# Optimization experiments

Hardware: AMD Instinct MI355X
Metric: run time of the kernel (lower is better)

## Reference

```python
import jax, jax.numpy as jnp
import numpy as np

TIME_GAP_BUCKETS = 64
B, L, H, MAX_T = 256, 200, 256, 256
VOCAB, N_GROUPS = 50000, 16
EPS = 1e-5


def setup_inputs() -> dict:
    key = jax.random.key(0)
    ks = jax.random.split(key, 16)
    lengths = jax.random.randint(ks[0], (B,), 0, L + 1)
    mask = jnp.arange(L)[None, :] < lengths[:, None]

    def toks(k, hi):  # jagged padded-dense: zeros past each row's length
        return jnp.where(mask, jax.random.randint(k, (B, L), 0, hi), 0)

    inp = {
        'history_tokens': toks(ks[1], VOCAB),
        'history_post_tokens': toks(ks[2], VOCAB),
        'history_author_tokens': toks(ks[3], VOCAB),
        'history_action_tokens': toks(ks[4], VOCAB),
        'history_time_gap': toks(ks[5], TIME_GAP_BUCKETS + 1),
        'history_group_ids': jnp.where(mask, jnp.sort(jax.random.randint(ks[6], (B, L), 1, N_GROUPS + 1), axis=1), 0),
        'lengths': lengths,
    }
    s = 0.02
    inp['token_emb'] = jax.random.normal(ks[7], (VOCAB, H)) * s
    inp['ln_gamma'] = jnp.ones((6 * H,))
    inp['ln_beta'] = jnp.zeros((6 * H,))
    inp['w1'] = jax.random.normal(ks[8], (6 * H, 4 * H)) * (1.0 / np.sqrt(6 * H)).astype(np.float32)
    inp['b1'] = jnp.zeros((4 * H,))
    inp['w2'] = jax.random.normal(ks[9], (4 * H, H)) * (1.0 / np.sqrt(4 * H)).astype(np.float32)
    inp['b2'] = jnp.zeros((H,))
    inp['time_gap_emb'] = (jax.random.normal(ks[10], (TIME_GAP_BUCKETS + 1, H)) * s).at[0].set(0.0)  # padding_idx=0
    inp['group_emb'] = (jax.random.normal(ks[11], (N_GROUPS + 1, H)) * s).at[0].set(0.0)  # padding_idx=0
    inp['pos_emb'] = jax.random.normal(ks[12], (MAX_T, H)) * s
    inp['sep_token'] = jax.random.normal(ks[13], (H,)) * 0.02
    return inp


def _layernorm(x, g, b):
    mu = jnp.mean(x, axis=-1, keepdims=True)
    var = jnp.mean(jnp.square(x - mu), axis=-1, keepdims=True)
    return (x - mu) * jax.lax.rsqrt(var + EPS) * g + b


def _merge_with_sep(event_tokens, group_ids, mask, sep_token):
    # mask is a prefix mask (positions < lengths), so valid tokens are contiguous.
    Bn, Ln, Hn = event_tokens.shape
    next_mask = jnp.pad(mask[:, 1:], ((0, 0), (0, 1)))
    next_group = jnp.pad(group_ids[:, 1:], ((0, 0), (0, 1)))
    sep_after = mask & next_mask & (group_ids != next_group)  # insert sep after token i
    seps_before = jnp.cumsum(sep_after, axis=1) - sep_after.astype(jnp.int32)  # exclusive scan
    token_pos = jnp.arange(Ln)[None, :] + seps_before  # position within merged piece list
    total = mask.sum(axis=1) + sep_after.sum(axis=1)  # [B] merged piece count
    offset = MAX_T - total  # right-align; negative -> leading pieces dropped
    tok_idx = offset[:, None] + token_pos
    sep_idx = tok_idx + 1
    tok_idx = jnp.where(mask & (tok_idx >= 0), tok_idx, MAX_T)  # MAX_T => dropped
    sep_idx = jnp.where(sep_after & (sep_idx >= 0), sep_idx, MAX_T)
    sep_rows = jnp.broadcast_to(sep_token, (Ln, Hn))

    def scatter_one(ev, ti, si):
        buf = jnp.zeros((MAX_T, Hn), ev.dtype)
        buf = buf.at[ti].set(ev, mode='drop')
        buf = buf.at[si].set(sep_rows, mode='drop')
        return buf

    merged = jax.vmap(scatter_one)(event_tokens, tok_idx, sep_idx)
    merged_len = jnp.minimum(total, MAX_T)
    merged_mask = jnp.arange(MAX_T)[None, :] >= (MAX_T - merged_len)[:, None]
    return merged, merged_mask


def reference(history_tokens, history_post_tokens, history_author_tokens,
              history_action_tokens, history_time_gap, history_group_ids,
              lengths, token_emb, ln_gamma, ln_beta, w1, b1, w2, b2,
              time_gap_emb, group_emb, pos_emb, sep_token):
    mask = jnp.arange(L)[None, :] < lengths[:, None]
    hh = token_emb[history_tokens]
    ph = token_emb[history_post_tokens]
    ah = token_emb[history_author_tokens]
    ch = token_emb[history_action_tokens]
    th = time_gap_emb[jnp.clip(history_time_gap, 0, TIME_GAP_BUCKETS)]
    gh = group_emb[history_group_ids]
    ev = jnp.concatenate([hh, ph, ah, ch, th, gh], axis=-1)  # [B, L, 6H]
    x = _layernorm(ev, ln_gamma, ln_beta)
    x = jax.nn.silu(x @ w1 + b1)  # dropout is identity in eval mode
    event_tokens = x @ w2 + b2  # [B, L, H]
    merged, mm = _merge_with_sep(event_tokens, history_group_ids, mask, sep_token)
    merged = (merged + pos_emb[None]) * mm[..., None].astype(merged.dtype)
    return merged, mm
```

## Files before the change

### kernel.cpp

```cpp
#include <hip/hip_runtime.h>
#include <hip/hip_bf16.h>
#include <math.h>

#define B_    256
#define L_    200
#define H_    256
#define MAXT  256
#define SIXH  1536
#define FOURH 1024
#define NPOS  (B_ * L_)

typedef __attribute__((ext_vector_type(8))) short short8;
typedef __attribute__((ext_vector_type(4))) float f32x4;

typedef __attribute__((address_space(3))) void lds_void;
typedef const __attribute__((address_space(1))) void gbl_void;

#define ASM_BAR() asm volatile("s_barrier" ::: "memory")
#define VMCNT4()  asm volatile("s_waitcnt vmcnt(4)" ::: "memory")
#define VMCNT0()  asm volatile("s_waitcnt vmcnt(0)" ::: "memory")

__global__ void fused_pre(const int* __restrict__ lengths,
                          const int* __restrict__ gids,
                          int* __restrict__ offsets,
                          int* __restrict__ tpos,
                          __hip_bfloat16* __restrict__ x) {
  int b = blockIdx.x, t = threadIdx.x;
  int lane = t & 63, wv = t >> 6;

  int len_t = lengths[t];
  int s = len_t;
#pragma unroll
  for (int o = 1; o < 64; o <<= 1) {
    int v = __shfl_up(s, o);
    if (lane >= o) s += v;
  }
  __shared__ int wsum[4];
  __shared__ int all_off[257];
  if (lane == 63) wsum[wv] = s;
  __syncthreads();
  int pre = 0;
#pragma unroll
  for (int k = 0; k < 4; k++)
    if (k < wv) pre += wsum[k];
  s += pre;
  all_off[t] = s - len_t;
  if (t == 255) all_off[256] = s;
  __syncthreads();

  int base = all_off[b];
  int total = all_off[256];
  if (t == 0) {
    offsets[b] = base;
    if (b == 0) offsets[B_] = total;
  }

  __shared__ int g[L_];
  int len = lengths[b];
  for (int l = t; l < len; l += 256) g[l] = gids[b * L_ + l];
  __syncthreads();
  if (t == 0) {
    int nsep = 0;
    for (int l = 0; l + 1 < len; l++)
      if (g[l] != g[l + 1]) nsep++;
    int tot = len + nsep;
    int off = MAXT - tot;
    int sb = 0;
    for (int l = 0; l < len; l++) {
      int ti = off + l + sb;
      tpos[base + l] = (ti >= 0) ? (b * MAXT + ti) : -1;
      if (l + 1 < len && g[l] != g[l + 1]) sb++;
    }
  }

  int padded = (total + 255) & ~255;
  int row = total + b;
  if (row < padded) {
#pragma unroll
    for (int j = 0; j < 6; j++)
      x[(size_t)row * SIXH + j * 256 + t] = __float2bfloat16(0.0f);
  }
}

__global__ void transpose_both(const float* __restrict__ w1,
                               __hip_bfloat16* __restrict__ w1t,
                               const float* __restrict__ w2,
                               __hip_bfloat16* __restrict__ w2t) {
  __shared__ float tile[32][33];
  int id = blockIdx.x;
  const float* in; __hip_bfloat16* out; int R, C, tc, tr;
  if (id < 1536) {
    in = w1; out = w1t; R = 1536; C = 1024; tc = id & 31; tr = id >> 5;
  } else {
    int j = id - 1536;
    in = w2; out = w2t; R = 1024; C = 256; tc = j & 7; tr = j >> 3;
  }
  int tx = threadIdx.x & 31, ty = threadIdx.x >> 5;
#pragma unroll
  for (int i = 0; i < 4; i++)
    tile[ty + i * 8][tx] = in[(size_t)(tr * 32 + ty + i * 8) * C + tc * 32 + tx];
  __syncthreads();
#pragma unroll
  for (int i = 0; i < 4; i++)
    out[(size_t)(tc * 32 + ty + i * 8) * R + tr * 32 + tx] =
        __float2bfloat16(tile[tx][ty + i * 8]);
}

__global__ void embed_ln_kernel(const int* __restrict__ tok0,
                                const int* __restrict__ tok1,
                                const int* __restrict__ tok2,
                                const int* __restrict__ tok3,
                                const int* __restrict__ tgap,
                                const int* __restrict__ gid,
                                const int* __restrict__ lengths,
                                const int* __restrict__ offsets,
                                const float* __restrict__ token_emb,
                                const float* __restrict__ tg_emb,
                                const float* __restrict__ g_emb,
                                const float* __restrict__ gamma,
                                const float* __restrict__ beta,
                                __hip_bfloat16* __restrict__ xout) {
  int l = blockIdx.x, b = blockIdx.y;
  if (l >= lengths[b]) return;
  int pos = b * L_ + l;
  int row = offsets[b] + l;
  int t = threadIdx.x;
  int wv = t >> 6;
  int ln = t & 63;
  int c4 = ln * 4;

  const float* tab;
  int idx;
  if (wv == 0)      { tab = token_emb; idx = tok0[pos]; }
  else if (wv == 1) { tab = token_emb; idx = tok1[pos]; }
  else if (wv == 2) { tab = token_emb; idx = tok2[pos]; }
  else if (wv == 3) { tab = token_emb; idx = tok3[pos]; }
  else if (wv == 4) { tab = tg_emb;    idx = min(max(tgap[pos], 0), 64); }
  else              { tab = g_emb;     idx = gid[pos]; }

  float4 v = *(const float4*)&tab[(size_t)idx * H_ + c4];

  float s = v.x + v.y + v.z + v.w;
  float q = v.x * v.x + v.y * v.y + v.z * v.z + v.w * v.w;
#pragma unroll
  for (int o = 32; o; o >>= 1) { s += __shfl_down(s, o); q += __shfl_down(q, o); }
  __shared__ float ps[6], pq[6];
  if (ln == 0) { ps[wv] = s; pq[wv] = q; }
  __syncthreads();
  float ts = 0.f, tq = 0.f;
#pragma unroll
  for (int k = 0; k < 6; k++) { ts += ps[k]; tq += pq[k]; }
  float mu = ts * (1.0f / 1536.0f);
  float var = tq * (1.0f / 1536.0f) - mu * mu;
  float rstd = rsqrtf(var + 1e-5f);

  int cbase = wv * 256 + c4;
  float4 gm = *(const float4*)&gamma[cbase];
  float4 bt = *(const float4*)&beta[cbase];
  float y0 = (v.x - mu) * rstd * gm.x + bt.x;
  float y1 = (v.y - mu) * rstd * gm.y + bt.y;
  float y2 = (v.z - mu) * rstd * gm.z + bt.z;
  float y3 = (v.w - mu) * rstd * gm.w + bt.w;
  __hip_bfloat16 h0 = __float2bfloat16(y0), h1 = __float2bfloat16(y1);
  __hip_bfloat16 h2 = __float2bfloat16(y2), h3 = __float2bfloat16(y3);
  ushort4 pk;
  pk.x = *(unsigned short*)&h0; pk.y = *(unsigned short*)&h1;
  pk.z = *(unsigned short*)&h2; pk.w = *(unsigned short*)&h3;
  *(ushort4*)&xout[(size_t)row * SIXH + cbase] = pk;
}

__global__ __launch_bounds__(512, 2)
void gemm1_8ph(const __hip_bfloat16* __restrict__ A,
               const __hip_bfloat16* __restrict__ Bt,
               const float* __restrict__ bias,
               __hip_bfloat16* __restrict__ out,
               const int* __restrict__ total_ptr) {
  constexpr int K = SIXH;
  constexpr int NT = K / 64;
  constexpr int N = FOURH;

  extern __shared__ __align__(16) char lds[];

  int total = total_ptr[0];
  int padded = (total + 255) & ~255;
  int num_mt = padded >> 8;

  int bid = blockIdx.x;
  int xcd = bid & 7;
  int slot = bid >> 3;
  int nt = slot & 3;
  int mtb = slot >> 2;
  int n0 = nt * 256;

  int tid = threadIdx.x;
  int lane = tid & 63;
  int w = tid >> 6;
  int wave_m = w >> 2;
  int wave_n = w & 3;

  int r15 = lane & 15, g = lane >> 4;
  int slot_r = (((r15 & 1) << 2) | g) ^ (r15 >> 1);
  int lane_off = (r15 >> 1) * 128 + slot_r * 16;

  int s0 = (tid & 7) ^ ((tid >> 3) & 7);
  int scol = (s0 & 3) * 8;
  int row0 = ((tid >> 3) << 1) + (s0 >> 2);
  int ldst0 = w * 1024;

  float bv4[4];
#pragma unroll
  for (int ni = 0; ni < 4; ni++)
    bv4[ni] = bias[n0 + wave_n * 64 + ni * 16 + r15];

#define REGA(d, h) (lds + (d) * 65536 + (h) * 16384)
#define REGB(d, h) (lds + (d) * 65536 + 32768 + (h) * 16384)

#define STAGE(P, t0, kt, h, rb)                                                \
  do {                                                                         \
    __builtin_amdgcn_global_load_lds(                                          \
        (gbl_void*)((P) + (size_t)((t0) + row0) * K + (kt) * 64 + (h) * 32 +   \
                    scol),                                                     \
        (lds_void*)((rb) + ldst0), 16, 0, 0);                                  \
    __builtin_amdgcn_global_load_lds(                                          \
        (gbl_void*)((P) + (size_t)((t0) + row0 + 128) * K + (kt) * 64 +        \
                    (h) * 32 + scol),                                          \
        (lds_void*)((rb) + 8192 + ldst0), 16, 0, 0);                           \
  } while (0)

  for (int mt = xcd + 8 * mtb; mt < num_mt; mt += 64) {
    int m0 = mt * 256;

    f32x4 acc[8][4] = {};

    STAGE(A, m0, 0, 0, REGA(0, 0));
    STAGE(Bt, n0, 0, 0, REGB(0, 0));
    STAGE(A, m0, 0, 1, REGA(0, 1));
    STAGE(Bt, n0, 0, 1, REGB(0, 1));
    STAGE(A, m0, 1, 0, REGA(1, 0));
    STAGE(Bt, n0, 1, 0, REGB(1, 0));
    VMCNT4();
    ASM_BAR();

    for (int kt = 0; kt < NT; ++kt) {
      int d = kt & 1;
      int kc1 = (kt + 1 < NT) ? kt + 1 : NT - 1;
      int kc2 = (kt + 2 < NT) ? kt + 2 : NT - 1;
      char* A0 = REGA(d, 0); char* A1 = REGA(d, 1);
      char* B0 = REGB(d, 0); char* B1 = REGB(d, 1);
      char* An1 = REGA(d ^ 1, 1);
      char* Bn1 = REGB(d ^ 1, 1);

      short8 a[4], b[4];

#pragma unroll
      for (int ni = 0; ni < 4; ni++)
        b[ni] = *(const short8*)(B0 + (wave_n * 64 + ni * 16) * 64 + lane_off);
#pragma unroll
      for (int j = 0; j < 4; j++)
        a[j] = *(const short8*)(A0 + (wave_m * 128 + j * 16) * 64 + lane_off);
      STAGE(A, m0, kc1, 1, An1);
      __builtin_amdgcn_s_setprio(1);
#pragma unroll
      for (int j = 0; j < 4; j++)
#pragma unroll
        for (int ni = 0; ni < 4; ni++)
          acc[j][ni] = __builtin_amdgcn_mfma_f32_16x16x32_bf16(a[j], b[ni],
                                                               acc[j][ni], 0, 0, 0);
      __builtin_amdgcn_s_setprio(0);
#pragma unroll
      for (int j = 0; j < 4; j++)
        a[j] = *(const short8*)(A0 + (wave_m * 128 + (4 + j) * 16) * 64 + lane_off);
      STAGE(Bt, n0, kc1, 1, Bn1);
      __builtin_amdgcn_s_setprio(1);
#pragma unroll
      for (int j = 0; j < 4; j++)
#pragma unroll
        for (int ni = 0; ni < 4; ni++)
          acc[4 + j][ni] = __builtin_amdgcn_mfma_f32_16x16x32_bf16(
              a[j], b[ni], acc[4 + j][ni], 0, 0, 0);
      __builtin_amdgcn_s_setprio(0);
      ASM_BAR();

#pragma unroll
      for (int ni = 0; ni < 4; ni++)
        b[ni] = *(const short8*)(B1 + (wave_n * 64 + ni * 16) * 64 + lane_off);
#pragma unroll
      for (int j = 0; j < 4; j++)
        a[j] = *(const short8*)(A1 + (wave_m * 128 + j * 16) * 64 + lane_off);
      STAGE(A, m0, kc2, 0, A0);
      __builtin_amdgcn_s_setprio(1);
#pragma unroll
      for (int j = 0; j < 4; j++)
#pragma unroll
        for (int ni = 0; ni < 4; ni++)
          acc[j][ni] = __builtin_amdgcn_mfma_f32_16x16x32_bf16(a[j], b[ni],
                                                               acc[j][ni], 0, 0, 0);
      __builtin_amdgcn_s_setprio(0);
#pragma unroll
      for (int j = 0; j < 4; j++)
        a[j] = *(const short8*)(A1 + (wave_m * 128 + (4 + j) * 16) * 64 + lane_off);
      STAGE(Bt, n0, kc2, 0, B0);
      __builtin_amdgcn_s_setprio(1);
#pragma unroll
      for (int j = 0; j < 4; j++)
#pragma unroll
        for (int ni = 0; ni < 4; ni++)
          acc[4 + j][ni] = __builtin_amdgcn_mfma_f32_16x16x32_bf16(
              a[j], b[ni], acc[4 + j][ni], 0, 0, 0);
      __builtin_amdgcn_s_setprio(0);
      VMCNT4();
      ASM_BAR();
    }
    VMCNT0();

    int r0 = g * 4;
#pragma unroll
    for (int mi = 0; mi < 8; mi++)
#pragma unroll
      for (int ni = 0; ni < 4; ni++) {
        int col = n0 + wave_n * 64 + ni * 16 + r15;
        float bv = bv4[ni];
#pragma unroll
        for (int r = 0; r < 4; r++) {
          int row = m0 + wave_m * 128 + mi * 16 + r0 + r;
          float v = acc[mi][ni][r] + bv;
          v = v / (1.0f + __expf(-v));
          out[(size_t)row * N + col] = __float2bfloat16(v);
        }
      }
  }
#undef STAGE
#undef REGA
#undef REGB
}

__global__ __launch_bounds__(512, 2)
void gemm2_wide(const __hip_bfloat16* __restrict__ A,
                const __hip_bfloat16* __restrict__ Bt,
                const float* __restrict__ bias,
                const int* __restrict__ tpos,
                const float* __restrict__ pos_emb,
                float* __restrict__ out,
                const int* __restrict__ total_ptr) {
  constexpr int K = FOURH;
  int m0 = blockIdx.x * 128;
  int total = total_ptr[0];
  int padded = (total + 127) & ~127;
  if (m0 >= padded) return;

  __shared__ __hip_bfloat16 As[128 * 64];
  __shared__ __hip_bfloat16 Bs[256 * 64];
  int tid = threadIdx.x;
  int lane = tid & 63, w = tid >> 6;
  int wave_m = w >> 2;
  int wave_n = w & 3;
  int wm = wave_m * 64, wn = wave_n * 64;

  int srow = lane >> 3;
  int scol = (lane & 7) * 8;
  int r15 = lane & 15, g = lane >> 4;

  f32x4 acc[4][4] = {};

  for (int k0 = 0; k0 < K; k0 += 64) {
#pragma unroll
    for (int i = 0; i < 2; i++) {
      int c = w * 2 + i;
      int row = c * 8 + srow;
      __builtin_amdgcn_global_load_lds(
          (gbl_void*)&A[(size_t)(m0 + row) * K + k0 + scol],
          (lds_void*)(As + c * 512), 16, 0, 0);
    }
#pragma unroll
    for (int i = 0; i < 4; i++) {
      int c = w * 4 + i;
      int row = c * 8 + srow;
      __builtin_amdgcn_global_load_lds(
          (gbl_void*)&Bt[(size_t)row * K + k0 + scol],
          (lds_void*)(Bs + c * 512), 16, 0, 0);
    }
    __syncthreads();
#pragma unroll
    for (int kk = 0; kk < 64; kk += 32) {
      short8 a[4], bb[4];
#pragma unroll
      for (int m = 0; m < 4; m++)
        a[m] = *(const short8*)&As[(wm + m * 16 + r15) * 64 + kk + 8 * g];
#pragma unroll
      for (int n = 0; n < 4; n++)
        bb[n] = *(const short8*)&Bs[(wn + n * 16 + r15) * 64 + kk + 8 * g];
#pragma unroll
      for (int m = 0; m < 4; m++)
#pragma unroll
        for (int n = 0; n < 4; n++)
          acc[m][n] = __builtin_amdgcn_mfma_f32_16x16x32_bf16(a[m], bb[n],
                                                              acc[m][n], 0, 0, 0);
    }
    __syncthreads();
  }

  int r0 = g * 4;
#pragma unroll
  for (int m = 0; m < 4; m++) {
#pragma unroll
    for (int r = 0; r < 4; r++) {
      int row = m0 + wm + m * 16 + r0 + r;
      if (row >= total) continue;
      int pa = tpos[row];
      if (pa < 0) continue;
      int p = pa & (MAXT - 1);
#pragma unroll
      for (int n = 0; n < 4; n++) {
        int col = wn + n * 16 + r15;
        float v = acc[m][n][r] + bias[col] + pos_emb[p * H_ + col];
        out[(size_t)pa * H_ + col] = v;
      }
    }
  }
}

__global__ void merge2_kernel(const int* __restrict__ gids,
                              const int* __restrict__ lengths,
                              const float* __restrict__ sep_token,
                              const float* __restrict__ pos_emb,
                              float* __restrict__ out) {
  int b = blockIdx.x, t = threadIdx.x;
  __shared__ signed char src[MAXT];
  __shared__ int g[L_];
  __shared__ int sh_total;
  int len = lengths[b];
  src[t] = 0;
  for (int l = t; l < len; l += 256) g[l] = gids[b * L_ + l];
  __syncthreads();
  if (t == 0) {
    int nsep = 0;
    for (int l = 0; l + 1 < len; l++)
      if (g[l] != g[l + 1]) nsep++;
    int total = len + nsep;
    sh_total = total;
    int off = MAXT - total;
    int sb = 0;
    for (int l = 0; l < len; l++) {
      int ti = off + l + sb;
      if (ti >= 0) src[ti] = 2;
      if (l + 1 < len && g[l] != g[l + 1]) {
        if (ti + 1 >= 0) src[ti + 1] = 1;
        sb++;
      }
    }
  }
  __syncthreads();
  int total = sh_total;
  int mlen = min(total, MAXT);

  int q = t >> 6, lane = t & 63, c4 = lane * 4;
  float4 sep4 = *(const float4*)&sep_token[c4];
  float* orow = out + (size_t)b * MAXT * H_;
  for (int p0 = 0; p0 < MAXT; p0 += 4) {
    int p = p0 + q;
    int s = src[p];
    if (s == 2) continue;
    float4 v;
    if (s == 1) {
      float4 pe = *(const float4*)&pos_emb[p * H_ + c4];
      v.x = sep4.x + pe.x; v.y = sep4.y + pe.y;
      v.z = sep4.z + pe.z; v.w = sep4.w + pe.w;
    } else {
      v.x = 0.f; v.y = 0.f; v.z = 0.f; v.w = 0.f;
    }
    *(float4*)&orow[(size_t)p * H_ + c4] = v;
  }
  float* mm = out + (size_t)B_ * MAXT * H_;
  mm[b * MAXT + t] = (t >= MAXT - mlen) ? 1.0f : 0.0f;
}

extern "C" void kernel_launch(void* const* d_in, const int* in_sizes, int n_in,
                              void* d_out, int out_size, void* d_ws,
                              size_t ws_size, hipStream_t stream) {
  const int* tok0 = (const int*)d_in[0];
  const int* tok1 = (const int*)d_in[1];
  const int* tok2 = (const int*)d_in[2];
  const int* tok3 = (const int*)d_in[3];
  const int* tgap = (const int*)d_in[4];
  const int* gid  = (const int*)d_in[5];
  const int* lengths = (const int*)d_in[6];
  const float* token_emb = (const float*)d_in[7];
  const float* gamma = (const float*)d_in[8];
  const float* beta  = (const float*)d_in[9];
  const float* w1 = (const float*)d_in[10];
  const float* b1 = (const float*)d_in[11];
  const float* w2 = (const float*)d_in[12];
  const float* b2 = (const float*)d_in[13];
  const float* tg_emb = (const float*)d_in[14];
  const float* g_emb  = (const float*)d_in[15];
  const float* pos_emb = (const float*)d_in[16];
  const float* sep_tok = (const float*)d_in[17];

  const size_t NEEDED = 266019844;
  if (ws_size < NEEDED) return;

  char* ws = (char*)d_ws;
  __hip_bfloat16* x = (__hip_bfloat16*)ws;
  __hip_bfloat16* h = (__hip_bfloat16*)(ws + 157286400);
  __hip_bfloat16* w1t = (__hip_bfloat16*)(ws + 262144000);
  __hip_bfloat16* w2t = (__hip_bfloat16*)(ws + 265289728);
  int* offsets = (int*)(ws + 265814016);
  int* tpos = (int*)(ws + 265815044);

  fused_pre<<<B_, 256, 0, stream>>>(lengths, gid, offsets, tpos, x);

  transpose_both<<<1792, 256, 0, stream>>>(w1, w1t, w2, w2t);

  embed_ln_kernel<<<dim3(L_, B_), 384, 0, stream>>>(
      tok0, tok1, tok2, tok3, tgap, gid, lengths, offsets, token_emb, tg_emb,
      g_emb, gamma, beta, x);

  hipFuncSetAttribute((const void*)gemm1_8ph,
                      hipFuncAttributeMaxDynamicSharedMemorySize, 131072);
  gemm1_8ph<<<256, 512, 131072, stream>>>(x, w1t, b1, h, offsets + B_);

  gemm2_wide<<<NPOS / 128, 512, 0, stream>>>(h, w2t, b2, tpos, pos_emb,
                                             (float*)d_out, offsets + B_);

  merge2_kernel<<<B_, 256, 0, stream>>>(gid, lengths, sep_tok, pos_emb,
                                        (float*)d_out);
}
```

Measured before the change: 252.5 us.

## Fuse embedding gather and LayerNorm into GEMM1 via algebraic LN folding

Removes the materialized normalized activation matrix. GEMM1 now gathers raw bf16 embedding rows directly into LDS by token index, and LayerNorm is applied in the epilogue as rstd*acc - mu*rstd*G + U. Here gamma is folded into W1 and the column sums of gamma*W1 and beta*W1 are precomputed. Per-row statistics come from per-table-row sum and sum-of-squares computed in a conversion pass over the 50000-row embedding table. This trades the x write/read traffic for a full-table conversion each call plus extra small kernels. The variance formula differs numerically, and LN is now applied to bf16-rounded inputs before the matmul rather than after.

After: 300.0 us. 1.19x slower.

```diff
diff --git a/kernel.cpp b/kernel.cpp
--- a/kernel.cpp
+++ b/kernel.cpp
@@ -9,6 +9,7 @@
 #define SIXH  1536
 #define FOURH 1024
 #define NPOS  (B_ * L_)
+#define PM    51456
 
 typedef __attribute__((ext_vector_type(8))) short short8;
 typedef __attribute__((ext_vector_type(4))) float f32x4;
@@ -20,11 +21,103 @@
 #define VMCNT4()  asm volatile("s_waitcnt vmcnt(4)" ::: "memory")
 #define VMCNT0()  asm volatile("s_waitcnt vmcnt(0)" ::: "memory")
 
+__global__ void conv_tables(const float* __restrict__ tok,
+                            const float* __restrict__ tgt,
+                            const float* __restrict__ gt,
+                            unsigned short* __restrict__ tokb,
+                            unsigned short* __restrict__ tgb,
+                            unsigned short* __restrict__ gb,
+                            float2* __restrict__ tok_st,
+                            float2* __restrict__ tg_st,
+                            float2* __restrict__ g_st) {
+  int bid = blockIdx.x, t = threadIdx.x;
+  const float* src; unsigned short* dst; float2* st; int row;
+  if (bid < 50000)      { src = tok; dst = tokb; st = tok_st; row = bid; }
+  else if (bid < 50065) { src = tgt; dst = tgb;  st = tg_st;  row = bid - 50000; }
+  else                  { src = gt;  dst = gb;   st = g_st;   row = bid - 50065; }
+
+  float4 v = ((const float4*)(src + (size_t)row * 256))[t];
+  __hip_bfloat16 h0 = __float2bfloat16(v.x), h1 = __float2bfloat16(v.y);
+  __hip_bfloat16 h2 = __float2bfloat16(v.z), h3 = __float2bfloat16(v.w);
+  ushort4 o;
+  o.x = *(unsigned short*)&h0; o.y = *(unsigned short*)&h1;
+  o.z = *(unsigned short*)&h2; o.w = *(unsigned short*)&h3;
+  ((ushort4*)(dst + (size_t)row * 256))[t] = o;
+
+  float s = v.x + v.y + v.z + v.w;
+  float q = v.x * v.x + v.y * v.y + v.z * v.z + v.w * v.w;
+#pragma unroll
+  for (int off = 32; off; off >>= 1) {
+    s += __shfl_down(s, off);
+    q += __shfl_down(q, off);
+  }
+  if (t == 0) st[row] = make_float2(s, q);
+}
+
+__global__ void transpose_both(const float* __restrict__ w1,
+                               __hip_bfloat16* __restrict__ w1t,
+                               const float* __restrict__ w2,
+                               __hip_bfloat16* __restrict__ w2t,
+                               const float* __restrict__ gamma) {
+  __shared__ float tile[32][33];
+  int id = blockIdx.x;
+  const float* in; __hip_bfloat16* out; int R, C, tc, tr;
+  bool isw1 = id < 1536;
+  if (isw1) {
+    in = w1; out = w1t; R = 1536; C = 1024; tc = id & 31; tr = id >> 5;
+  } else {
+    int j = id - 1536;
+    in = w2; out = w2t; R = 1024; C = 256; tc = j & 7; tr = j >> 3;
+  }
+  int tx = threadIdx.x & 31, ty = threadIdx.x >> 5;
+#pragma unroll
+  for (int i = 0; i < 4; i++)
+    tile[ty + i * 8][tx] = in[(size_t)(tr * 32 + ty + i * 8) * C + tc * 32 + tx];
+  __syncthreads();
+  float gm = isw1 ? gamma[tr * 32 + tx] : 1.0f;
+#pragma unroll
+  for (int i = 0; i < 4; i++)
+    out[(size_t)(tc * 32 + ty + i * 8) * R + tr * 32 + tx] =
+        __float2bfloat16(tile[tx][ty + i * 8] * gm);
+}
+
+__global__ void colstats(const float* __restrict__ w1,
+                         const float* __restrict__ gamma,
+                         const float* __restrict__ beta,
+                         float* __restrict__ Gn, float* __restrict__ Un) {
+  int t = threadIdx.x & 255;
+  int kq = threadIdx.x >> 8;
+  int n = blockIdx.x * 256 + t;
+  float G = 0.f, U = 0.f;
+  int k0 = kq * 384;
+  for (int k = k0; k < k0 + 384; k++) {
+    float w = w1[(size_t)k * 1024 + n];
+    G = fmaf(gamma[k], w, G);
+    U = fmaf(beta[k], w, U);
+  }
+  __shared__ float sG[4][256], sU[4][256];
+  sG[kq][t] = G; sU[kq][t] = U;
+  __syncthreads();
+  if (kq == 0) {
+    Gn[n] = sG[0][t] + sG[1][t] + sG[2][t] + sG[3][t];
+    Un[n] = sU[0][t] + sU[1][t] + sU[2][t] + sU[3][t];
+  }
+}
+
 __global__ void fused_pre(const int* __restrict__ lengths,
+                          const int* __restrict__ tok0,
+                          const int* __restrict__ tok1,
+                          const int* __restrict__ tok2,
+                          const int* __restrict__ tok3,
+                          const int* __restrict__ tgap,
                           const int* __restrict__ gids,
+                          const float2* __restrict__ tok_st,
+                          const float2* __restrict__ tg_st,
+                          const float2* __restrict__ g_st,
                           int* __restrict__ offsets,
                           int* __restrict__ tpos,
-                          __hip_bfloat16* __restrict__ x) {
+                          int* __restrict__ cidx,
+                          float2* __restrict__ lnp) {
   int b = blockIdx.x, t = threadIdx.x;
   int lane = t & 63, wv = t >> 6;
 
@@ -55,8 +148,31 @@
     if (b == 0) offsets[B_] = total;
   }
 
+  int len = lengths[b];
+
+  if (t < len) {
+    int pos = b * L_ + t;
+    int row = base + t;
+    int i0 = tok0[pos], i1 = tok1[pos], i2 = tok2[pos], i3 = tok3[pos];
+    int i4 = min(max(tgap[pos], 0), 64);
+    int i5 = gids[pos];
+    cidx[row] = i0;
+    cidx[PM + row] = i1;
+    cidx[2 * PM + row] = i2;
+    cidx[3 * PM + row] = i3;
+    cidx[4 * PM + row] = i4;
+    cidx[5 * PM + row] = i5;
+    float2 a0 = tok_st[i0], a1 = tok_st[i1], a2 = tok_st[i2], a3 = tok_st[i3];
+    float2 a4 = tg_st[i4], a5 = g_st[i5];
+    float S = a0.x + a1.x + a2.x + a3.x + a4.x + a5.x;
+    float Q = a0.y + a1.y + a2.y + a3.y + a4.y + a5.y;
+    float mu = S * (1.0f / 1536.0f);
+    float var = Q * (1.0f / 1536.0f) - mu * mu;
+    float rstd = rsqrtf(var + 1e-5f);
+    lnp[row] = make_float2(rstd, mu * rstd);
+  }
+
   __shared__ int g[L_];
-  int len = lengths[b];
   for (int l = t; l < len; l += 256) g[l] = gids[b * L_ + l];
   __syncthreads();
   if (t == 0) {
@@ -71,110 +187,28 @@
       tpos[base + l] = (ti >= 0) ? (b * MAXT + ti) : -1;
       if (l + 1 < len && g[l] != g[l + 1]) sb++;
     }
-  }
-
-  int padded = (total + 255) & ~255;
-  int row = total + b;
-  if (row < padded) {
-#pragma unroll
-    for (int j = 0; j < 6; j++)
-      x[(size_t)row * SIXH + j * 256 + t] = __float2bfloat16(0.0f);
-  }
-}
-
-__global__ void transpose_both(const float* __restrict__ w1,
-                               __hip_bfloat16* __restrict__ w1t,
-                               const float* __restrict__ w2,
-                               __hip_bfloat16* __restrict__ w2t) {
-  __shared__ float tile[32][33];
-  int id = blockIdx.x;
-  const float* in; __hip_bfloat16* out; int R, C, tc, tr;
-  if (id < 1536) {
-    in = w1; out = w1t; R = 1536; C = 1024; tc = id & 31; tr = id >> 5;
-  } else {
-    int j = id - 1536;
-    in = w2; out = w2t; R = 1024; C = 256; tc = j & 7; tr = j >> 3;
-  }
-  int tx = threadIdx.x & 31, ty = threadIdx.x >> 5;
-#pragma unroll
-  for (int i = 0; i < 4; i++)
-    tile[ty + i * 8][tx] = in[(size_t)(tr * 32 + ty + i * 8) * C + tc * 32 + tx];
-  __syncthreads();
-#pragma unroll
-  for (int i = 0; i < 4; i++)
-    out[(size_t)(tc * 32 + ty + i * 8) * R + tr * 32 + tx] =
-        __float2bfloat16(tile[tx][ty + i * 8]);
-}
-
-__global__ void embed_ln_kernel(const int* __restrict__ tok0,
-                                const int* __restrict__ tok1,
-                                const int* __restrict__ tok2,
-                                const int* __restrict__ tok3,
-                                const int* __restrict__ tgap,
-                                const int* __restrict__ gid,
-                                const int* __restrict__ lengths,
-                                const int* __restrict__ offsets,
-                                const float* __restrict__ token_emb,
-                                const float* __restrict__ tg_emb,
-                                const float* __restrict__ g_emb,
-                                const float* __restrict__ gamma,
-                                const float* __restrict__ beta,
-                                __hip_bfloat16* __restrict__ xout) {
-  int l = blockIdx.x, b = blockIdx.y;
-  if (l >= lengths[b]) return;
-  int pos = b * L_ + l;
-  int row = offsets[b] + l;
-  int t = threadIdx.x;
-  int wv = t >> 6;
-  int ln = t & 63;
-  int c4 = ln * 4;
-
-  const float* tab;
-  int idx;
-  if (wv == 0)      { tab = token_emb; idx = tok0[pos]; }
-  else if (wv == 1) { tab = token_emb; idx = tok1[pos]; }
-  else if (wv == 2) { tab = token_emb; idx = tok2[pos]; }
-  else if (wv == 3) { tab = token_emb; idx = tok3[pos]; }
-  else if (wv == 4) { tab = tg_emb;    idx = min(max(tgap[pos], 0), 64); }
-  else              { tab = g_emb;     idx = gid[pos]; }
-
-  float4 v = *(const float4*)&tab[(size_t)idx * H_ + c4];
-
-  float s = v.x + v.y + v.z + v.w;
-  float q = v.x * v.x + v.y * v.y + v.z * v.z + v.w * v.w;
-#pragma unroll
-  for (int o = 32; o; o >>= 1) { s += __shfl_down(s, o); q += __shfl_down(q, o); }
-  __shared__ float ps[6], pq[6];
-  if (ln == 0) { ps[wv] = s; pq[wv] = q; }
-  __syncthreads();
-  float ts = 0.f, tq = 0.f;
-#pragma unroll
-  for (int k = 0; k < 6; k++) { ts += ps[k]; tq += pq[k]; }
-  float mu = ts * (1.0f / 1536.0f);
-  float var = tq * (1.0f / 1536.0f) - mu * mu;
-  float rstd = rsqrtf(var + 1e-5f);
-
-  int cbase = wv * 256 + c4;
-  float4 gm = *(const float4*)&gamma[cbase];
-  float4 bt = *(const float4*)&beta[cbase];
-  float y0 = (v.x - mu) * rstd * gm.x + bt.x;
-  float y1 = (v.y - mu) * rstd * gm.y + bt.y;
-  float y2 = (v.z - mu) * rstd * gm.z + bt.z;
-  float y3 = (v.w - mu) * rstd * gm.w + bt.w;
-  __hip_bfloat16 h0 = __float2bfloat16(y0), h1 = __float2bfloat16(y1);
-  __hip_bfloat16 h2 = __float2bfloat16(y2), h3 = __float2bfloat16(y3);
-  ushort4 pk;
-  pk.x = *(unsigned short*)&h0; pk.y = *(unsigned short*)&h1;
-  pk.z = *(unsigned short*)&h2; pk.w = *(unsigned short*)&h3;
-  *(ushort4*)&xout[(size_t)row * SIXH + cbase] = pk;
+    int padded = (total + 255) & ~255;
+    int prow = total + b;
+    if (prow < padded) {
+#pragma unroll
+      for (int j = 0; j < 6; j++) cidx[j * PM + prow] = 0;
+      lnp[prow] = make_float2(0.f, 0.f);
+    }
+  }
 }
 
 __global__ __launch_bounds__(512, 2)
-void gemm1_8ph(const __hip_bfloat16* __restrict__ A,
-               const __hip_bfloat16* __restrict__ Bt,
-               const float* __restrict__ bias,
-               __hip_bfloat16* __restrict__ out,
-               const int* __restrict__ total_ptr) {
+void gemm1_fused(const unsigned short* __restrict__ tokb,
+                 const unsigned short* __restrict__ tgb,
+                 const unsigned short* __restrict__ gb,
+                 const int* __restrict__ cidx,
+                 const float2* __restrict__ lnp,
+                 const __hip_bfloat16* __restrict__ Bt,
+                 const float* __restrict__ Gn,
+                 const float* __restrict__ Un,
+                 const float* __restrict__ bias,
+                 __hip_bfloat16* __restrict__ out,
+                 const int* __restrict__ total_ptr) {
   constexpr int K = SIXH;
   constexpr int NT = K / 64;
   constexpr int N = FOURH;
@@ -207,22 +241,38 @@
   int row0 = ((tid >> 3) << 1) + (s0 >> 2);
   int ldst0 = w * 1024;
 
-  float bv4[4];
-#pragma unroll
-  for (int ni = 0; ni < 4; ni++)
-    bv4[ni] = bias[n0 + wave_n * 64 + ni * 16 + r15];
+  float Gc[4], Uc[4];
+#pragma unroll
+  for (int ni = 0; ni < 4; ni++) {
+    int col = n0 + wave_n * 64 + ni * 16 + r15;
+    Gc[ni] = Gn[col];
+    Uc[ni] = Un[col] + bias[col];
+  }
 
 #define REGA(d, h) (lds + (d) * 65536 + (h) * 16384)
 #define REGB(d, h) (lds + (d) * 65536 + 32768 + (h) * 16384)
 
-#define STAGE(P, t0, kt, h, rb)                                                \
+#define STAGE_A(kc, h, rb)                                                     \
+  do {                                                                         \
+    const unsigned short* _tb =                                                \
+        ((kc) >> 2) < 4 ? tokb : (((kc) >> 2) == 4 ? tgb : gb);                \
+    size_t _off = (size_t)(((kc) & 3) * 128 + (h) * 64 + scol * 2);            \
+    __builtin_amdgcn_global_load_lds(                                          \
+        (gbl_void*)((const char*)_tb + (size_t)c0[(kc) >> 2] * 512 + _off),    \
+        (lds_void*)((rb) + ldst0), 16, 0, 0);                                  \
+    __builtin_amdgcn_global_load_lds(                                          \
+        (gbl_void*)((const char*)_tb + (size_t)c1[(kc) >> 2] * 512 + _off),    \
+        (lds_void*)((rb) + 8192 + ldst0), 16, 0, 0);                           \
+  } while (0)
+
+#define STAGE_B(kt, h, rb)                                                     \
   do {                                                                         \
     __builtin_amdgcn_global_load_lds(                                          \
-        (gbl_void*)((P) + (size_t)((t0) + row0) * K + (kt) * 64 + (h) * 32 +   \
+        (gbl_void*)(Bt + (size_t)(n0 + row0) * K + (kt) * 64 + (h) * 32 +      \
                     scol),                                                     \
         (lds_void*)((rb) + ldst0), 16, 0, 0);                                  \
     __builtin_amdgcn_global_load_lds(                                          \
-        (gbl_void*)((P) + (size_t)((t0) + row0 + 128) * K + (kt) * 64 +        \
+        (gbl_void*)(Bt + (size_t)(n0 + row0 + 128) * K + (kt) * 64 +           \
                     (h) * 32 + scol),                                          \
         (lds_void*)((rb) + 8192 + ldst0), 16, 0, 0);                           \
   } while (0)
@@ -230,17 +280,25 @@
   for (int mt = xcd + 8 * mtb; mt < num_mt; mt += 64) {
     int m0 = mt * 256;
 
+    int c0[6], c1[6];
+#pragma unroll
+    for (int j = 0; j < 6; j++) {
+      c0[j] = cidx[j * PM + m0 + row0];
+      c1[j] = cidx[j * PM + m0 + row0 + 128];
+    }
+
     f32x4 acc[8][4] = {};
 
-    STAGE(A, m0, 0, 0, REGA(0, 0));
-    STAGE(Bt, n0, 0, 0, REGB(0, 0));
-    STAGE(A, m0, 0, 1, REGA(0, 1));
-    STAGE(Bt, n0, 0, 1, REGB(0, 1));
-    STAGE(A, m0, 1, 0, REGA(1, 0));
-    STAGE(Bt, n0, 1, 0, REGB(1, 0));
+    STAGE_A(0, 0, REGA(0, 0));
+    STAGE_B(0, 0, REGB(0, 0));
+    STAGE_A(0, 1, REGA(0, 1));
+    STAGE_B(0, 1, REGB(0, 1));
+    STAGE_A(1, 0, REGA(1, 0));
+    STAGE_B(1, 0, REGB(1, 0));
     VMCNT4();
     ASM_BAR();
 
+#pragma unroll
     for (int kt = 0; kt < NT; ++kt) {
       int d = kt & 1;
       int kc1 = (kt + 1 < NT) ? kt + 1 : NT - 1;
@@ -258,7 +316,7 @@
 #pragma unroll
       for (int j = 0; j < 4; j++)
         a[j] = *(const short8*)(A0 + (wave_m * 128 + j * 16) * 64 + lane_off);
-      STAGE(A, m0, kc1, 1, An1);
+      STAGE_A(kc1, 1, An1);
       __builtin_amdgcn_s_setprio(1);
 #pragma unroll
       for (int j = 0; j < 4; j++)
@@ -270,7 +328,7 @@
 #pragma unroll
       for (int j = 0; j < 4; j++)
         a[j] = *(const short8*)(A0 + (wave_m * 128 + (4 + j) * 16) * 64 + lane_off);
-      STAGE(Bt, n0, kc1, 1, Bn1);
+      STAGE_B(kc1, 1, Bn1);
       __builtin_amdgcn_s_setprio(1);
 #pragma unroll
       for (int j = 0; j < 4; j++)
@@ -287,7 +345,7 @@
 #pragma unroll
       for (int j = 0; j < 4; j++)
         a[j] = *(const short8*)(A1 + (wave_m * 128 + j * 16) * 64 + lane_off);
-      STAGE(A, m0, kc2, 0, A0);
+      STAGE_A(kc2, 0, A0);
       __builtin_amdgcn_s_setprio(1);
 #pragma unroll
       for (int j = 0; j < 4; j++)
@@ -299,7 +357,7 @@
 #pragma unroll
       for (int j = 0; j < 4; j++)
         a[j] = *(const short8*)(A1 + (wave_m * 128 + (4 + j) * 16) * 64 + lane_off);
-      STAGE(Bt, n0, kc2, 0, B0);
+      STAGE_B(kc2, 0, B0);
       __builtin_amdgcn_s_setprio(1);
 #pragma unroll
       for (int j = 0; j < 4; j++)
@@ -313,23 +371,24 @@
     }
     VMCNT0();
 
-    int r0 = g * 4;
+    int r0g = g * 4;
 #pragma unroll
     for (int mi = 0; mi < 8; mi++)
 #pragma unroll
-      for (int ni = 0; ni < 4; ni++) {
-        int col = n0 + wave_n * 64 + ni * 16 + r15;
-        float bv = bv4[ni];
-#pragma unroll
-        for (int r = 0; r < 4; r++) {
-          int row = m0 + wave_m * 128 + mi * 16 + r0 + r;
-          float v = acc[mi][ni][r] + bv;
+      for (int r = 0; r < 4; r++) {
+        int row = m0 + wave_m * 128 + mi * 16 + r0g + r;
+        float2 lp = lnp[row];
+#pragma unroll
+        for (int ni = 0; ni < 4; ni++) {
+          int col = n0 + wave_n * 64 + ni * 16 + r15;
+          float v = acc[mi][ni][r] * lp.x - lp.y * Gc[ni] + Uc[ni];
           v = v / (1.0f + __expf(-v));
           out[(size_t)row * N + col] = __float2bfloat16(v);
         }
       }
   }
-#undef STAGE
+#undef STAGE_A
+#undef STAGE_B
 #undef REGA
 #undef REGB
 }
@@ -496,28 +555,41 @@
   const float* pos_emb = (const float*)d_in[16];
   const float* sep_tok = (const float*)d_in[17];
 
-  const size_t NEEDED = 266019844;
+  const size_t NEEDED = 136432384;
   if (ws_size < NEEDED) return;
 
   char* ws = (char*)d_ws;
-  __hip_bfloat16* x = (__hip_bfloat16*)ws;
-  __hip_bfloat16* h = (__hip_bfloat16*)(ws + 157286400);
-  __hip_bfloat16* w1t = (__hip_bfloat16*)(ws + 262144000);
-  __hip_bfloat16* w2t = (__hip_bfloat16*)(ws + 265289728);
-  int* offsets = (int*)(ws + 265814016);
-  int* tpos = (int*)(ws + 265815044);
-
-  fused_pre<<<B_, 256, 0, stream>>>(lengths, gid, offsets, tpos, x);
-
-  transpose_both<<<1792, 256, 0, stream>>>(w1, w1t, w2, w2t);
-
-  embed_ln_kernel<<<dim3(L_, B_), 384, 0, stream>>>(
-      tok0, tok1, tok2, tok3, tgap, gid, lengths, offsets, token_emb, tg_emb,
-      g_emb, gamma, beta, x);
-
-  hipFuncSetAttribute((const void*)gemm1_8ph,
+  __hip_bfloat16* h = (__hip_bfloat16*)ws;
+  __hip_bfloat16* w1t = (__hip_bfloat16*)(ws + 104857600);
+  __hip_bfloat16* w2t = (__hip_bfloat16*)(ws + 108003328);
+  unsigned short* tokb = (unsigned short*)(ws + 108527616);
+  unsigned short* tgb = (unsigned short*)(ws + 134127616);
+  unsigned short* gb = (unsigned short*)(ws + 134160896);
+  float2* tok_st = (float2*)(ws + 134169600);
+  float2* tg_st = (float2*)(ws + 134569600);
+  float2* g_st = (float2*)(ws + 134570240);
+  int* offsets = (int*)(ws + 134570496);
+  int* tpos = (int*)(ws + 134571776);
+  int* cidx = (int*)(ws + 134777600);
+  float2* lnp = (float2*)(ws + 136012544);
+  float* Gn = (float*)(ws + 136424192);
+  float* Un = (float*)(ws + 136428288);
+
+  conv_tables<<<50082, 64, 0, stream>>>(token_emb, tg_emb, g_emb, tokb, tgb,
+                                        gb, tok_st, tg_st, g_st);
+
+  transpose_both<<<1792, 256, 0, stream>>>(w1, w1t, w2, w2t, gamma);
+
+  colstats<<<4, 1024, 0, stream>>>(w1, gamma, beta, Gn, Un);
+
+  fused_pre<<<B_, 256, 0, stream>>>(lengths, tok0, tok1, tok2, tok3, tgap,
+                                    gid, tok_st, tg_st, g_st, offsets, tpos,
+                                    cidx, lnp);
+
+  hipFuncSetAttribute((const void*)gemm1_fused,
                       hipFuncAttributeMaxDynamicSharedMemorySize, 131072);
-  gemm1_8ph<<<256, 512, 131072, stream>>>(x, w1t, b1, h, offsets + B_);
+  gemm1_fused<<<256, 512, 131072, stream>>>(tokb, tgb, gb, cidx, lnp, w1t, Gn,
+                                            Un, b1, h, offsets + B_);
 
   gemm2_wide<<<NPOS / 128, 512, 0, stream>>>(h, w2t, b2, tpos, pos_emb,
                                              (float*)d_out, offsets + B_);
```
